# Kernel optimization log

Measured on AMD Instinct MI355X. Metric: run time of the kernel, lower is better.

The kernel has to match this reference:

```python
import jax, jax.numpy as jnp
import numpy as np

B, L, H = 16, 1024, 128
HEADS = 8
DK = H // HEADS
CONV_LAYERS, KERNEL = 4, 7
PAD = KERNEL // 2
NEG = -1e30
EPS = 1e-5


def setup_inputs() -> dict:
    key = jax.random.key(0)
    ks = jax.random.split(key, 12)
    s = 0.05
    emb = jax.random.normal(ks[0], (B, L, H), jnp.float32)
    # valid-prefix mask (QANet-style padding mask): lengths in [L//2, L]
    lengths = jax.random.randint(ks[1], (B,), L // 2, L + 1)
    mask = (jnp.arange(L)[None, :] < lengths[:, None]).astype(jnp.int32)
    depth_w = jax.random.normal(ks[2], (CONV_LAYERS, H, 1, KERNEL), jnp.float32) * s
    depth_b = jax.random.normal(ks[3], (CONV_LAYERS, H), jnp.float32) * s
    pt_w = jax.random.normal(ks[4], (CONV_LAYERS, H, H), jnp.float32) * s
    pt_b = jax.random.normal(ks[5], (CONV_LAYERS, H), jnp.float32) * s
    wq = jax.random.normal(ks[6], (HEADS, DK, H), jnp.float32) * s
    wk = jax.random.normal(ks[7], (HEADS, DK, H), jnp.float32) * s
    wv = jax.random.normal(ks[8], (HEADS, DK, H), jnp.float32) * s
    wo = jax.random.normal(ks[9], (H, HEADS * DK), jnp.float32) * s
    wff = jax.random.normal(ks[10], (H, H), jnp.float32) * s
    return dict(emb=emb, mask=mask, depth_w=depth_w, depth_b=depth_b,
                pt_w=pt_w, pt_b=pt_b, wq=wq, wk=wk, wv=wv, wo=wo, wff=wff)


def layer_norm(x):
    # fresh nn.LayerNorm each fwd: gamma=1, beta=0, eps=1e-5, biased variance
    m = jnp.mean(x, axis=-1, keepdims=True)
    v = jnp.mean(jnp.square(x - m), axis=-1, keepdims=True)
    return (x - m) * jax.lax.rsqrt(v + EPS)


def depth_sep_conv(x, dw, db, pw, pb):
    # x: [B,L,C]; depthwise conv1d (groups=C) then pointwise 1x1 conv
    xc = x.transpose(0, 2, 1)  # [B,C,L]
    out = jax.lax.conv_general_dilated(
        xc, dw, window_strides=(1,), padding=[(PAD, PAD)],
        feature_group_count=dw.shape[0],
        dimension_numbers=("NCH", "OIH", "NCH"))
    out = out + db[None, :, None]
    out = jnp.einsum("bcl,oc->bol", out, pw) + pb[None, :, None]
    return out.transpose(0, 2, 1)  # [B,L,H]


def att_block(x, mask, wq, wk, wv, wo):
    # x: [B,L,H]; per-batch prefix block mask of size nsum x nsum,
    # and scaling by sqrt(nsum) (faithful to the original, NOT sqrt(dk))
    nsum = mask.sum(-1)  # [B]
    valid = jnp.arange(x.shape[1])[None, :] < nsum[:, None]  # [B,L]
    nmask = (valid[:, :, None] & valid[:, None, :]).astype(x.dtype)[:, None]  # [B,1,L,L]
    q = jnp.einsum("blc,hdc->bhld", x, wq)
    k = jnp.einsum("blc,hdc->bhld", x, wk)
    v = jnp.einsum("blc,hdc->bhld", x, wv)
    scale = jnp.sqrt(nsum.astype(jnp.float32))[:, None, None, None]
    logits = jnp.einsum("bhld,bhmd->bhlm", q, k) / scale
    logits = nmask * logits + (1.0 - nmask) * NEG  # masked_softmax
    p = jax.nn.softmax(logits, axis=-1)
    o = jnp.einsum("bhlm,bhmd->bhld", p, v)
    o = o.transpose(0, 2, 1, 3).reshape(x.shape[0], x.shape[1], HEADS * DK)
    return o @ wo.T


def reference(emb, mask, depth_w, depth_b, pt_w, pt_b, wq, wk, wv, wo, wff):
    out = emb
    for i in range(CONV_LAYERS):
        out = out + depth_sep_conv(layer_norm(out), depth_w[i], depth_b[i], pt_w[i], pt_b[i])
    out = out + att_block(layer_norm(out), mask, wq, wk, wv, wo)
    out = out + layer_norm(out) @ wff.T
    return out
```

## Files before the change

kernel.cpp:

```cpp
#include <hip/hip_runtime.h>

typedef unsigned short u16;
typedef float f32x4 __attribute__((ext_vector_type(4)));
typedef unsigned int u32x4 __attribute__((ext_vector_type(4)));
typedef unsigned short u16x4 __attribute__((ext_vector_type(4)));
typedef unsigned short u16x8 __attribute__((ext_vector_type(8)));
typedef __bf16 bf16x8 __attribute__((ext_vector_type(8)));

#define DEVFN static __device__ __forceinline__

DEVFN float bf2f(u16 u) {
    unsigned int i = ((unsigned int)u) << 16;
    float f;
    __builtin_memcpy(&f, &i, 4);
    return f;
}
DEVFN u16 f2bf(float f) {
    __bf16 h = (__bf16)f;
    return __builtin_bit_cast(u16, h);
}

DEVFN bf16x8 ldb(const u16* p) { return __builtin_bit_cast(bf16x8, *(const u16x8*)p); }

DEVFN void stage8(u16* dst, const float* src) {
    float4 a = *(const float4*)src;
    float4 b = *(const float4*)(src + 4);
    u16x8 m;
    m[0] = f2bf(a.x); m[1] = f2bf(a.y); m[2] = f2bf(a.z); m[3] = f2bf(a.w);
    m[4] = f2bf(b.x); m[5] = f2bf(b.y); m[6] = f2bf(b.z); m[7] = f2bf(b.w);
    *(u16x8*)dst = m;
}

DEVFN f32x4 mfma16(bf16x8 a, bf16x8 b, f32x4 c) {
    return __builtin_amdgcn_mfma_f32_16x16x32_bf16(a, b, c, 0, 0, 0);
}

#if __has_builtin(__builtin_amdgcn_exp2f)
DEVFN float ex2(float x) { return __builtin_amdgcn_exp2f(x); }
#else
DEVFN float ex2(float x) { return exp2f(x); }
#endif

DEVFN void ln_stats(float4 v, float& mean, float& rs) {
    float s = (v.x + v.y) + (v.z + v.w);
    float q = v.x * v.x + v.y * v.y + v.z * v.z + v.w * v.w;
#pragma unroll
    for (int off = 1; off < 32; off <<= 1) {
        s += __shfl_xor(s, off);
        q += __shfl_xor(q, off);
    }
    mean = s * (1.0f / 128.0f);
    float var = q * (1.0f / 128.0f) - mean * mean;
    rs = rsqrtf(var + 1e-5f);
}
DEVFN u16x4 ln_pack(float4 v, float mean, float rs) {
    u16x4 o;
    o[0] = f2bf((v.x - mean) * rs);
    o[1] = f2bf((v.y - mean) * rs);
    o[2] = f2bf((v.z - mean) * rs);
    o[3] = f2bf((v.w - mean) * rs);
    return o;
}

__global__ __launch_bounds__(512) void k_convstack(const float* __restrict__ x,
                                                   const float* __restrict__ ptw,
                                                   const float* __restrict__ dwAll,
                                                   const float* __restrict__ dbAll,
                                                   const float* __restrict__ pbAll,
                                                   const float* __restrict__ wq,
                                                   const float* __restrict__ wk,
                                                   const float* __restrict__ wv,
                                                   const int* __restrict__ mask,
                                                   float* __restrict__ dst,
                                                   u16* __restrict__ qb,
                                                   u16* __restrict__ kb,
                                                   u16* __restrict__ vb) {
    __shared__ alignas(16) float sCur[56 * 128];
    __shared__ alignas(16) u16 sLC[64 * 128];
    __shared__ alignas(16) u16 sW[128 * 128];
    __shared__ int sred[8];
    int tid = threadIdx.x;
    int w = tid >> 6, l64 = tid & 63;
    int sub = l64 >> 5, l32 = l64 & 31;
    int b = blockIdx.x >> 5, lt = blockIdx.x & 31;
    int l0 = lt << 5;
    const float* xb = x + ((size_t)(b << 10)) * 128;
    float* dstb = dst + ((size_t)(b << 10)) * 128;
    int row16 = l64 & 15, g = l64 >> 4;
    f32x4 zf = {0.f, 0.f, 0.f, 0.f};

    {
        int2 mm = *(const int2*)&mask[(b << 10) + (tid << 1)];
        int part = mm.x + mm.y;
#pragma unroll
        for (int off = 1; off < 64; off <<= 1) part += __shfl_xor(part, off);
        if (l64 == 0) sred[w] = part;
    }

    for (int j = 0; j < 4; j++) {
        int lo = 3 * j;
        int hi = 56 - 3 * j;
        int cstart = lo + 3;
        int width = 50 - 6 * j;

        for (int r = lo + (w << 1) + sub; r < hi; r += 16) {
            int al = l0 - 12 + r;
            bool ok = (al >= 0) && (al < 1024);
            float4 v = {0.f, 0.f, 0.f, 0.f};
            if (ok) {
                if (j == 0) v = *(const float4*)&xb[(size_t)al * 128 + (l32 << 2)];
                else        v = *(const float4*)&sCur[r * 128 + (l32 << 2)];
            }
            if (j == 0) *(float4*)&sCur[r * 128 + (l32 << 2)] = v;
            float mean, rs;
            ln_stats(v, mean, rs);
            u16x4 pk = {0, 0, 0, 0};
            if (ok) pk = ln_pack(v, mean, rs);
            *(u16x4*)&sLC[r * 128 + (l32 << 2)] = pk;
        }
        __syncthreads();

        const float* Wp = ptw + j * 16384;
#pragma unroll
        for (int i = 0; i < 4; i++) {
            int e = i * 512 + tid;
            int r = e >> 4, cc = e & 15;
            stage8(&sW[r * 128 + ((cc ^ (r & 15)) << 3)], &Wp[(r << 7) + (cc << 3)]);
        }

        int cp = l64;
        const float* dwp = dwAll + j * 896;
        float w0[7], w1[7];
#pragma unroll
        for (int k = 0; k < 7; k++) {
            w0[k] = dwp[(cp * 2) * 7 + k];
            w1[k] = dwp[(cp * 2 + 1) * 7 + k];
        }
        float b0 = dbAll[j * 128 + cp * 2], b1 = dbAll[j * 128 + cp * 2 + 1];
        int base = cstart + w * 7;
        float v0[13], v1[13];
#pragma unroll
        for (int k = 0; k < 13; k++) {
            int rw = base - 3 + k;
            rw = rw < 63 ? rw : 63;
            unsigned int pk = *(const unsigned int*)&sLC[rw * 128 + (cp << 1)];
            v0[k] = bf2f((u16)(pk & 0xffffu));
            v1[k] = bf2f((u16)(pk >> 16));
        }
        float a0[7], a1[7];
#pragma unroll
        for (int rr = 0; rr < 7; rr++) {
            float s0 = b0, s1 = b1;
#pragma unroll
            for (int k = 0; k < 7; k++) {
                s0 += v0[rr + k] * w0[k];
                s1 += v1[rr + k] * w1[k];
            }
            a0[rr] = s0;
            a1[rr] = s1;
        }
        __syncthreads();

#pragma unroll
        for (int rr = 0; rr < 7; rr++) {
            int rel = w * 7 + rr;
            float s0 = (rel < width) ? a0[rr] : 0.0f;
            float s1 = (rel < width) ? a1[rr] : 0.0f;
            int cc = cp >> 2;
            *(unsigned int*)&sLC[rel * 128 + ((cc ^ (rel & 15)) << 3) + ((cp & 3) << 1)] =
                (unsigned int)f2bf(s0) | ((unsigned int)f2bf(s1) << 16);
        }
        *(unsigned int*)&sLC[(56 + w) * 128 + (l64 << 1)] = 0;
        __syncthreads();

        int mh = w >> 1, nh = w & 1;
        f32x4 acc[4] = {zf, zf, zf, zf};
#pragma unroll
        for (int kk = 0; kk < 4; kk++) {
            int chunk = ((kk * 4 + g) ^ row16) << 3;
            bf16x8 a = ldb(&sLC[(mh * 16 + row16) * 128 + chunk]);
#pragma unroll
            for (int n = 0; n < 4; n++) {
                bf16x8 bfr = ldb(&sW[(nh * 64 + n * 16 + row16) * 128 + chunk]);
                acc[n] = mfma16(a, bfr, acc[n]);
            }
        }
        const float* pbp = pbAll + j * 128;
#pragma unroll
        for (int n = 0; n < 4; n++) {
            int col = nh * 64 + n * 16 + row16;
            float bi = pbp[col];
#pragma unroll
            for (int r = 0; r < 4; r++) {
                int rel = mh * 16 + g * 4 + r;
                if (rel < width) {
                    int idx = cstart + rel;
                    float val = acc[n][r] + bi + sCur[idx * 128 + col];
                    sCur[idx * 128 + col] = val;
                    if (j == 3) dstb[(size_t)(l0 + rel) * 128 + col] = val;
                }
            }
        }
        __syncthreads();
    }

#pragma unroll
    for (int i = 0; i < 4; i++) {
        int e = i * 512 + tid;
        int r = e >> 4, cc = e & 15;
        stage8(&sW[r * 128 + ((cc ^ (r & 15)) << 3)], &wq[(r << 7) + (cc << 3)]);
    }

    int nsum = 0;
#pragma unroll
    for (int i = 0; i < 8; i++) nsum += sred[i];
    float qs = rsqrtf((float)nsum) * 1.44269504089f;

#pragma unroll
    for (int rp = 0; rp < 2; rp++) {
        int r = rp * 16 + (w << 1) + sub;
        float4 v = *(const float4*)&sCur[(12 + r) * 128 + (l32 << 2)];
        float mean, rs;
        ln_stats(v, mean, rs);
        u16x4 pk = ln_pack(v, mean, rs);
        int cc = l32 >> 1;
        *(u16x4*)&sLC[r * 128 + ((cc ^ (r & 15)) << 3) + ((l32 & 1) << 2)] = pk;
    }

    int mh = w >> 2, nh = w & 3;
#pragma unroll
    for (int y = 0; y < 3; y++) {
        u16* dsty = (y == 0) ? qb : (y == 1) ? kb : vb;
        float sc = (y == 0) ? qs : 1.0f;
        if (y > 0) {
            const float* Wy = (y == 1) ? wk : wv;
            __syncthreads();
#pragma unroll
            for (int i = 0; i < 4; i++) {
                int e = i * 512 + tid;
                int r = e >> 4, cc = e & 15;
                stage8(&sW[r * 128 + ((cc ^ (r & 15)) << 3)], &Wy[(r << 7) + (cc << 3)]);
            }
        }
        __syncthreads();
        f32x4 acc[2] = {zf, zf};
#pragma unroll
        for (int kk = 0; kk < 4; kk++) {
            int chunk = ((kk * 4 + g) ^ row16) << 3;
            bf16x8 a = ldb(&sLC[(mh * 16 + row16) * 128 + chunk]);
#pragma unroll
            for (int n = 0; n < 2; n++) {
                bf16x8 bfr = ldb(&sW[(nh * 32 + n * 16 + row16) * 128 + chunk]);
                acc[n] = mfma16(a, bfr, acc[n]);
            }
        }
#pragma unroll
        for (int n = 0; n < 2; n++) {
            int col = nh * 32 + n * 16 + row16;
#pragma unroll
            for (int r = 0; r < 4; r++) {
                int row = l0 + mh * 16 + g * 4 + r;
                dsty[((size_t)(b << 10) + row) * 128 + col] = f2bf(acc[n][r] * sc);
            }
        }
    }
}

__global__ __launch_bounds__(256) void k_wolnff(const u16* __restrict__ X,
                                                const float* __restrict__ wo,
                                                const float* __restrict__ wff,
                                                const float* __restrict__ res,
                                                float* __restrict__ dst) {
    __shared__ alignas(16) u16 sX[64 * 128];
    __shared__ alignas(16) u16 sW1[128 * 128];
    __shared__ alignas(16) u16 sW2[128 * 128];
    int tid = threadIdx.x;
    int w = tid >> 6, l64 = tid & 63;
    int rbase = blockIdx.x * 64;
#pragma unroll
    for (int j = 0; j < 8; j++) {
        int e = j * 256 + tid;
        int r = e >> 4, cc = e & 15;
        int sw = ((cc ^ (r & 15)) << 3);
        stage8(&sW1[r * 128 + sw], &wo[(r << 7) + (cc << 3)]);
        stage8(&sW2[r * 128 + sw], &wff[(r << 7) + (cc << 3)]);
    }
#pragma unroll
    for (int j = 0; j < 4; j++) {
        int e = j * 256 + tid;
        int r = e >> 4, cc = e & 15;
        *(u32x4*)&sX[r * 128 + ((cc ^ (r & 15)) << 3)] =
            *(const u32x4*)&X[((rbase + r) << 7) + (cc << 3)];
    }
    __syncthreads();

    int row16 = l64 & 15, g = l64 >> 4;
    f32x4 zf = {0.f, 0.f, 0.f, 0.f};
    f32x4 acc[8];
#pragma unroll
    for (int n = 0; n < 8; n++) acc[n] = zf;
#pragma unroll
    for (int kk = 0; kk < 4; kk++) {
        int chunk = ((kk * 4 + g) ^ row16) << 3;
        bf16x8 a = ldb(&sX[(w * 16 + row16) * 128 + chunk]);
#pragma unroll
        for (int n = 0; n < 8; n++) {
            bf16x8 bfr = ldb(&sW1[(n * 16 + row16) * 128 + chunk]);
            acc[n] = mfma16(a, bfr, acc[n]);
        }
    }
    f32x4 vals[8];
#pragma unroll
    for (int n = 0; n < 8; n++) {
        int col = n * 16 + row16;
#pragma unroll
        for (int r = 0; r < 4; r++)
            vals[n][r] = acc[n][r] + res[(size_t)(rbase + w * 16 + g * 4 + r) * 128 + col];
    }
    float mean[4], rstd[4];
#pragma unroll
    for (int r = 0; r < 4; r++) {
        float s = 0.f, q = 0.f;
#pragma unroll
        for (int n = 0; n < 8; n++) {
            s += vals[n][r];
            q += vals[n][r] * vals[n][r];
        }
#pragma unroll
        for (int off = 1; off < 16; off <<= 1) {
            s += __shfl_xor(s, off);
            q += __shfl_xor(q, off);
        }
        mean[r] = s * (1.0f / 128.0f);
        float var = q * (1.0f / 128.0f) - mean[r] * mean[r];
        rstd[r] = rsqrtf(var + 1e-5f);
    }
    __syncthreads();
#pragma unroll
    for (int n = 0; n < 8; n++) {
        int col = n * 16 + row16;
        int cc = col >> 3;
#pragma unroll
        for (int r = 0; r < 4; r++) {
            int row = w * 16 + g * 4 + r;
            sX[row * 128 + ((cc ^ (row & 15)) << 3) + (row16 & 7)] =
                f2bf((vals[n][r] - mean[r]) * rstd[r]);
        }
    }
    __syncthreads();
    f32x4 acc2[8];
#pragma unroll
    for (int n = 0; n < 8; n++) acc2[n] = zf;
#pragma unroll
    for (int kk = 0; kk < 4; kk++) {
        int chunk = ((kk * 4 + g) ^ row16) << 3;
        bf16x8 a = ldb(&sX[(w * 16 + row16) * 128 + chunk]);
#pragma unroll
        for (int n = 0; n < 8; n++) {
            bf16x8 bfr = ldb(&sW2[(n * 16 + row16) * 128 + chunk]);
            acc2[n] = mfma16(a, bfr, acc2[n]);
        }
    }
#pragma unroll
    for (int n = 0; n < 8; n++) {
        int col = n * 16 + row16;
#pragma unroll
        for (int r = 0; r < 4; r++)
            dst[(size_t)(rbase + w * 16 + g * 4 + r) * 128 + col] = vals[n][r] + acc2[n][r];
    }
}

#define LDVF(P)                                                                                \
    ({                                                                                         \
        const u16* vp_ = &sVt[row16 * 1032 + (P) * 32 + (g << 2)];                             \
        union { u16x4 h[2]; u16x8 v8; } uu_;                                                   \
        uu_.h[0] = *(const u16x4*)vp_;                                                         \
        uu_.h[1] = *(const u16x4*)(vp_ + 16);                                                  \
        __builtin_bit_cast(bf16x8, uu_.v8);                                                    \
    })

#define SM_PV(SV, VF)                                                                          \
    {                                                                                          \
        float p0 = ex2(SV[0]), p1 = ex2(SV[1]), p2 = ex2(SV[2]), p3 = ex2(SV[3]);              \
        float p4 = ex2(SV[4]), p5 = ex2(SV[5]), p6 = ex2(SV[6]), p7 = ex2(SV[7]);              \
        lrun += ((p0 + p1) + (p2 + p3)) + ((p4 + p5) + (p6 + p7));                             \
        bf16x8 pa = {(__bf16)p0, (__bf16)p1, (__bf16)p2, (__bf16)p3,                           \
                     (__bf16)p4, (__bf16)p5, (__bf16)p6, (__bf16)p7};                          \
        oacc = mfma16(VF, pa, oacc);                                                           \
    }

__global__ __launch_bounds__(512) void k_attn(const u16* __restrict__ Qg, const u16* __restrict__ Kg,
                                              const u16* __restrict__ Vg,
                                              const int* __restrict__ mask,
                                              u16* __restrict__ Og) {
    __shared__ alignas(16) u16 sVt[16 * 1032];
    __shared__ int sred[8];
    int tid = threadIdx.x;
    int w = tid >> 6, l = tid & 63;
    int bh = blockIdx.x >> 3;
    int qblk = blockIdx.x & 7;
    int b = bh >> 3, h = bh & 7;
    int row16 = l & 15, g = l >> 4;

    const u16* kg = Kg + (size_t)(b << 10) * 128 + (h << 4);
    const u16* vg = Vg + (size_t)(b << 10) * 128 + (h << 4);
#pragma unroll
    for (int j = 0; j < 4; j++) {
        int e = j * 512 + tid;
        int m = e >> 1, half = e & 1;
        u32x4 vv = *(const u32x4*)&vg[m * 128 + half * 8];
        union { u32x4 q; u16 s[8]; } u;
        u.q = vv;
#pragma unroll
        for (int jj = 0; jj < 8; jj++) sVt[(half * 8 + jj) * 1032 + m] = u.s[jj];
    }
    {
        int2 mm = *(const int2*)&mask[(b << 10) + (tid << 1)];
        int part = mm.x + mm.y;
#pragma unroll
        for (int off = 1; off < 64; off <<= 1) part += __shfl_xor(part, off);
        if (l == 0) sred[w] = part;
    }
    __syncthreads();
    int nsum = 0;
#pragma unroll
    for (int i = 0; i < 8; i++) nsum += sred[i];

    int qbase = qblk * 128 + w * 16;
    u16x8 z8 = {0, 0, 0, 0, 0, 0, 0, 0};
    const bf16x8 zb = __builtin_bit_cast(bf16x8, z8);
    f32x4 zf = {0.f, 0.f, 0.f, 0.f};

    bool rowv = (qbase + row16) < nsum;
    bf16x8 qf = zb;
    if (rowv && g < 2)
        qf = ldb(&Qg[(size_t)((b << 10) + qbase + row16) * 128 + (h << 4) + (g << 3)]);
    f32x4 oacc = zf;
    float lrun = 0.0f;

    const u16* kl = kg + row16 * 128 + (g << 3);
    int p = 0;
    if (qbase < nsum) {
        int full = nsum >> 5;
        bf16x8 ka0 = zb, ka1 = zb, kb0 = zb, kb1 = zb, vc = zb;
        if (full > 0) {
            if (g < 2) {
                ka0 = ldb(kl);
                ka1 = ldb(kl + 2048);
            }
            vc = LDVF(0);
        }
        if (full > 1 && g < 2) {
            kb0 = ldb(kl + 4096);
            kb1 = ldb(kl + 6144);
        }
        for (; p < full; p++) {
            bf16x8 kn0 = zb, kn1 = zb, vn = zb;
            if (p + 2 < full && g < 2) {
                kn0 = ldb(kl + 8192);
                kn1 = ldb(kl + 10240);
            }
            if (p + 1 < full) vn = LDVF(p + 1);
            kl += 4096;
            f32x4 s0 = mfma16(ka0, qf, zf);
            f32x4 s1 = mfma16(ka1, qf, zf);
            float sv[8];
#pragma unroll
            for (int r = 0; r < 4; r++) {
                sv[r] = s0[r];
                sv[4 + r] = s1[r];
            }
            SM_PV(sv, vc)
            ka0 = kb0; ka1 = kb1;
            kb0 = kn0; kb1 = kn1;
            vc = vn;
        }
        if (nsum & 31) {
            bf16x8 kf0 = zb, kf1 = zb;
            if (g < 2) {
                kf0 = ldb(kl);
                kf1 = ldb(kl + 2048);
            }
            bf16x8 vf = LDVF(p);
            int kb_ = p << 5;
            f32x4 s0 = mfma16(kf0, qf, zf);
            f32x4 s1 = mfma16(kf1, qf, zf);
            float negfill = rowv ? -1.0e30f : 0.0f;
            float sv[8];
#pragma unroll
            for (int r = 0; r < 4; r++) {
                sv[r] = ((kb_ + (g << 2) + r) < nsum) ? s0[r] : negfill;
                sv[4 + r] = ((kb_ + 16 + (g << 2) + r) < nsum) ? s1[r] : negfill;
            }
            SM_PV(sv, vf)
            p++;
        }
    }
    if (qbase + 16 > nsum && p < 32) {
        int ntail = 32 - p;
        __bf16 vcst = rowv ? (__bf16)0.0f : (__bf16)1.0f;
        bf16x8 pt = {vcst, vcst, vcst, vcst, vcst, vcst, vcst, vcst};
        if (!rowv) lrun += 8.0f * (float)ntail;
        for (; p < 32; p++) {
            bf16x8 vf = LDVF(p);
            oacc = mfma16(vf, pt, oacc);
        }
    }

    float lr = lrun;
    lr += __shfl_xor(lr, 16);
    lr += __shfl_xor(lr, 32);
    float inv = 1.0f / lr;
    u16x4 ov;
#pragma unroll
    for (int r = 0; r < 4; r++) ov[r] = f2bf(oacc[r] * inv);
    int q = qbase + row16;
    *(u16x4*)&Og[(size_t)((b << 10) + q) * 128 + (h << 4) + (g << 2)] = ov;
}

extern "C" void kernel_launch(void* const* d_in, const int* in_sizes, int n_in,
                              void* d_out, int out_size, void* d_ws, size_t ws_size,
                              hipStream_t stream) {
    const float* emb     = (const float*)d_in[0];
    const int*   mask    = (const int*)d_in[1];
    const float* depth_w = (const float*)d_in[2];
    const float* depth_b = (const float*)d_in[3];
    const float* pt_w    = (const float*)d_in[4];
    const float* pt_b    = (const float*)d_in[5];
    const float* wq      = (const float*)d_in[6];
    const float* wk      = (const float*)d_in[7];
    const float* wv      = (const float*)d_in[8];
    const float* wo      = (const float*)d_in[9];
    const float* wff     = (const float*)d_in[10];
    float* out = (float*)d_out;
    char* ws = (char*)d_ws;

    u16* qb    = (u16*)(ws + 8388608);
    u16* kb    = (u16*)(ws + 12582912);
    u16* vb    = (u16*)(ws + 16777216);
    u16* attnb = (u16*)(ws + 20971520);

    k_convstack<<<512, 512, 0, stream>>>(emb, pt_w, depth_w, depth_b, pt_b,
                                         wq, wk, wv, mask, out, qb, kb, vb);
    k_attn<<<1024, 512, 0, stream>>>(qb, kb, vb, mask, attnb);
    k_wolnff<<<256, 256, 0, stream>>>(attnb, wo, wff, out, out);
}
```

Before: 86.14 us.

## Process two query tiles per wave in attention to reuse K/V fragments

Each wave now handles 32 query rows (two 16-row tiles) instead of 16, so every K and V fragment loaded from global/LDS feeds two sets of MFMAs. The attention grid is halved (512 blocks), which cuts the redundant per-block V transpose into LDS and the mask reduction. In exchange, register pressure rises from the doubled accumulators and query fragments, and fewer blocks are available to fill the CUs. The masked-tail handling is extended so that rows past nsum still produce the uniform average of V.

```diff
diff --git a/kernel.cpp b/kernel.cpp
--- a/kernel.cpp
+++ b/kernel.cpp
@@ -379,14 +379,14 @@
         __builtin_bit_cast(bf16x8, uu_.v8);                                                    \
     })
 
-#define SM_PV(SV, VF)                                                                          \
+#define SM_PV(SV, VF, LR, OA)                                                                  \
     {                                                                                          \
         float p0 = ex2(SV[0]), p1 = ex2(SV[1]), p2 = ex2(SV[2]), p3 = ex2(SV[3]);              \
         float p4 = ex2(SV[4]), p5 = ex2(SV[5]), p6 = ex2(SV[6]), p7 = ex2(SV[7]);              \
-        lrun += ((p0 + p1) + (p2 + p3)) + ((p4 + p5) + (p6 + p7));                             \
+        LR += ((p0 + p1) + (p2 + p3)) + ((p4 + p5) + (p6 + p7));                               \
         bf16x8 pa = {(__bf16)p0, (__bf16)p1, (__bf16)p2, (__bf16)p3,                           \
                      (__bf16)p4, (__bf16)p5, (__bf16)p6, (__bf16)p7};                          \
-        oacc = mfma16(VF, pa, oacc);                                                           \
+        OA = mfma16(VF, pa, OA);                                                               \
     }
 
 __global__ __launch_bounds__(512) void k_attn(const u16* __restrict__ Qg, const u16* __restrict__ Kg,
@@ -397,8 +397,8 @@
     __shared__ int sred[8];
     int tid = threadIdx.x;
     int w = tid >> 6, l = tid & 63;
-    int bh = blockIdx.x >> 3;
-    int qblk = blockIdx.x & 7;
+    int bh = blockIdx.x >> 2;
+    int qblk = blockIdx.x & 3;
     int b = bh >> 3, h = bh & 7;
     int row16 = l & 15, g = l >> 4;
 
@@ -426,21 +426,27 @@
 #pragma unroll
     for (int i = 0; i < 8; i++) nsum += sred[i];
 
-    int qbase = qblk * 128 + w * 16;
+    int qbase0 = qblk * 256 + w * 32;
     u16x8 z8 = {0, 0, 0, 0, 0, 0, 0, 0};
     const bf16x8 zb = __builtin_bit_cast(bf16x8, z8);
     f32x4 zf = {0.f, 0.f, 0.f, 0.f};
 
-    bool rowv = (qbase + row16) < nsum;
-    bf16x8 qf = zb;
-    if (rowv && g < 2)
-        qf = ldb(&Qg[(size_t)((b << 10) + qbase + row16) * 128 + (h << 4) + (g << 3)]);
-    f32x4 oacc = zf;
-    float lrun = 0.0f;
+    bool rowv[2];
+    bf16x8 qf[2];
+    f32x4 oacc[2] = {zf, zf};
+    float lrun[2] = {0.0f, 0.0f};
+#pragma unroll
+    for (int t = 0; t < 2; t++) {
+        int q = qbase0 + t * 16 + row16;
+        rowv[t] = q < nsum;
+        qf[t] = zb;
+        if (rowv[t] && g < 2)
+            qf[t] = ldb(&Qg[(size_t)((b << 10) + q) * 128 + (h << 4) + (g << 3)]);
+    }
 
     const u16* kl = kg + row16 * 128 + (g << 3);
     int p = 0;
-    if (qbase < nsum) {
+    if (qbase0 < nsum) {
         int full = nsum >> 5;
         bf16x8 ka0 = zb, ka1 = zb, kb0 = zb, kb1 = zb, vc = zb;
         if (full > 0) {
@@ -462,15 +468,18 @@
             }
             if (p + 1 < full) vn = LDVF(p + 1);
             kl += 4096;
-            f32x4 s0 = mfma16(ka0, qf, zf);
-            f32x4 s1 = mfma16(ka1, qf, zf);
-            float sv[8];
-#pragma unroll
-            for (int r = 0; r < 4; r++) {
-                sv[r] = s0[r];
-                sv[4 + r] = s1[r];
-            }
-            SM_PV(sv, vc)
+#pragma unroll
+            for (int t = 0; t < 2; t++) {
+                f32x4 s0 = mfma16(ka0, qf[t], zf);
+                f32x4 s1 = mfma16(ka1, qf[t], zf);
+                float sv[8];
+#pragma unroll
+                for (int r = 0; r < 4; r++) {
+                    sv[r] = s0[r];
+                    sv[4 + r] = s1[r];
+                }
+                SM_PV(sv, vc, lrun[t], oacc[t])
+            }
             ka0 = kb0; ka1 = kb1;
             kb0 = kn0; kb1 = kn1;
             vc = vn;
@@ -483,39 +492,51 @@
             }
             bf16x8 vf = LDVF(p);
             int kb_ = p << 5;
-            f32x4 s0 = mfma16(kf0, qf, zf);
-            f32x4 s1 = mfma16(kf1, qf, zf);
-            float negfill = rowv ? -1.0e30f : 0.0f;
-            float sv[8];
-#pragma unroll
-            for (int r = 0; r < 4; r++) {
-                sv[r] = ((kb_ + (g << 2) + r) < nsum) ? s0[r] : negfill;
-                sv[4 + r] = ((kb_ + 16 + (g << 2) + r) < nsum) ? s1[r] : negfill;
-            }
-            SM_PV(sv, vf)
+#pragma unroll
+            for (int t = 0; t < 2; t++) {
+                f32x4 s0 = mfma16(kf0, qf[t], zf);
+                f32x4 s1 = mfma16(kf1, qf[t], zf);
+                float negfill = rowv[t] ? -1.0e30f : 0.0f;
+                float sv[8];
+#pragma unroll
+                for (int r = 0; r < 4; r++) {
+                    sv[r] = ((kb_ + (g << 2) + r) < nsum) ? s0[r] : negfill;
+                    sv[4 + r] = ((kb_ + 16 + (g << 2) + r) < nsum) ? s1[r] : negfill;
+                }
+                SM_PV(sv, vf, lrun[t], oacc[t])
+            }
             p++;
         }
     }
-    if (qbase + 16 > nsum && p < 32) {
+    bool act0 = (qbase0 + 16 > nsum);
+    bool act1 = (qbase0 + 32 > nsum);
+    if (act1 && p < 32) {
         int ntail = 32 - p;
-        __bf16 vcst = rowv ? (__bf16)0.0f : (__bf16)1.0f;
-        bf16x8 pt = {vcst, vcst, vcst, vcst, vcst, vcst, vcst, vcst};
-        if (!rowv) lrun += 8.0f * (float)ntail;
+        __bf16 c0 = rowv[0] ? (__bf16)0.0f : (__bf16)1.0f;
+        __bf16 c1 = rowv[1] ? (__bf16)0.0f : (__bf16)1.0f;
+        bf16x8 pt0 = {c0, c0, c0, c0, c0, c0, c0, c0};
+        bf16x8 pt1 = {c1, c1, c1, c1, c1, c1, c1, c1};
+        if (act0 && !rowv[0]) lrun[0] += 8.0f * (float)ntail;
+        if (!rowv[1]) lrun[1] += 8.0f * (float)ntail;
         for (; p < 32; p++) {
             bf16x8 vf = LDVF(p);
-            oacc = mfma16(vf, pt, oacc);
-        }
-    }
-
-    float lr = lrun;
-    lr += __shfl_xor(lr, 16);
-    lr += __shfl_xor(lr, 32);
-    float inv = 1.0f / lr;
-    u16x4 ov;
-#pragma unroll
-    for (int r = 0; r < 4; r++) ov[r] = f2bf(oacc[r] * inv);
-    int q = qbase + row16;
-    *(u16x4*)&Og[(size_t)((b << 10) + q) * 128 + (h << 4) + (g << 2)] = ov;
+            if (act0) oacc[0] = mfma16(vf, pt0, oacc[0]);
+            oacc[1] = mfma16(vf, pt1, oacc[1]);
+        }
+    }
+
+#pragma unroll
+    for (int t = 0; t < 2; t++) {
+        float lr = lrun[t];
+        lr += __shfl_xor(lr, 16);
+        lr += __shfl_xor(lr, 32);
+        float inv = 1.0f / lr;
+        u16x4 ov;
+#pragma unroll
+        for (int r = 0; r < 4; r++) ov[r] = f2bf(oacc[t][r] * inv);
+        int q = qbase0 + t * 16 + row16;
+        *(u16x4*)&Og[(size_t)((b << 10) + q) * 128 + (h << 4) + (g << 2)] = ov;
+    }
 }
 
 extern "C" void kernel_launch(void* const* d_in, const int* in_sizes, int n_in,
@@ -542,6 +563,6 @@
 
     k_convstack<<<512, 512, 0, stream>>>(emb, pt_w, depth_w, depth_b, pt_b,
                                          wq, wk, wv, mask, out, qb, kb, vb);
-    k_attn<<<1024, 512, 0, stream>>>(qb, kb, vb, mask, attnb);
+    k_attn<<<512, 512, 0, stream>>>(qb, kb, vb, mask, attnb);
     k_wolnff<<<256, 256, 0, stream>>>(attnb, wo, wff, out, out);
 }
```

After: 78.27 us, median of 3. -9.1%, faster.
